# Optimization experiments

Measured on AMD Instinct MI355X. Metric: run time of the kernel, lower is better.

The kernel has to match this reference:

```python
import jax, jax.numpy as jnp
import numpy as np

B, S, E, H = 4, 2048, 1024, 16
D = E // H  # head_dim = 64

def setup_inputs() -> dict:
    key = jax.random.key(0)
    k1, k2, k3 = jax.random.split(key, 3)
    x = jax.random.normal(k1, (B, S, E), dtype=jnp.float32)
    # nn.Linear(E, 3E, bias=False): y = x @ W^T; we store W already transposed as [E, 3E]
    w_qkv = jax.random.normal(k2, (E, 3 * E), dtype=jnp.float32) * (E ** -0.5)
    w_out = jax.random.normal(k3, (E, E), dtype=jnp.float32) * (E ** -0.5)
    b_out = jnp.zeros((E,), dtype=jnp.float32)
    return {"x": x, "w_qkv": w_qkv, "w_out": w_out, "b_out": b_out}

def reference(x, w_qkv, w_out, b_out):
    b, s, e = x.shape
    h, d = H, e // H
    # qkv projection then rearrange 'b s (qkv h d) -> qkv b h s d'
    qkv = (x @ w_qkv).reshape(b, s, 3, h, d).transpose(2, 0, 3, 1, 4)
    q, k, v = qkv[0], qkv[1], qkv[2]            # each [b, h, s, d]
    scale = jnp.asarray(d, x.dtype) ** -0.5
    att = jnp.einsum('bhxd,bhyd->bhxy', q, k) * scale   # [b, h, s, s]
    att = jax.nn.softmax(att, axis=-1)
    o = jnp.einsum('bhxy,bhyd->bhxd', att, v)           # [b, h, s, d]
    o = o.transpose(0, 2, 1, 3).reshape(b, s, e)        # 'b h s d -> b s (h d)'
    return o @ w_out + b_out
```

## Files before the change

### kernel.cpp

```cpp
#include <hip/hip_runtime.h>
#include <cstdint>
#include <cstddef>


typedef __attribute__((ext_vector_type(8))) short short8;
typedef __attribute__((ext_vector_type(4))) float float4_;
typedef unsigned int u32;
typedef unsigned short u16;

__device__ __forceinline__ u16 f2b(float f) {
  u32 u = __float_as_uint(f);
  u += 0x7FFFu + ((u >> 16) & 1u);
  return (u16)(u >> 16);
}

__device__ __forceinline__ float fexp2(float x) {
#if __has_builtin(__builtin_amdgcn_exp2f)
  return __builtin_amdgcn_exp2f(x);
#else
  return exp2f(x);
#endif
}

__device__ __forceinline__ u32 pk_trunc(float lo, float hi) {
#if __has_builtin(__builtin_amdgcn_perm)
  return __builtin_amdgcn_perm(__float_as_uint(hi), __float_as_uint(lo), 0x07060302);
#else
  return (__float_as_uint(hi) & 0xFFFF0000u) | (__float_as_uint(lo) >> 16);
#endif
}

#if __has_builtin(__builtin_amdgcn_fdot2_f32_bf16)
typedef __bf16 bf16x2 __attribute__((ext_vector_type(2)));
__device__ __forceinline__ float accum_pk(u32 pk, float acc) {
  bf16x2 p = __builtin_bit_cast(bf16x2, pk);
  bf16x2 one = __builtin_bit_cast(bf16x2, (u32)0x3F803F80u);
  return __builtin_amdgcn_fdot2_f32_bf16(p, one, acc, false);
}
#else
__device__ __forceinline__ float accum_pk(u32 pk, float acc) {
  return acc + __uint_as_float(pk << 16) + __uint_as_float(pk & 0xFFFF0000u);
}
#endif

__device__ __forceinline__ void async_cp16(const void* g, void* l) {
  __builtin_amdgcn_global_load_lds(
      (const __attribute__((address_space(1))) u32*)g,
      (__attribute__((address_space(3))) u32*)l, 16, 0, 0);
}


__device__ __forceinline__ void transpose_block(const float* __restrict__ in,
                                                u16* __restrict__ out,
                                                int R, int C, int bx, int by,
                                                float t[32][33]) {
  int tx = threadIdx.x & 31, ty = threadIdx.x >> 5;
  int r0 = by * 32, c0 = bx * 32;
#pragma unroll
  for (int k = 0; k < 4; k++)
    t[ty + 8 * k][tx] = in[(size_t)(r0 + ty + 8 * k) * C + c0 + tx];
  __syncthreads();
#pragma unroll
  for (int k = 0; k < 4; k++)
    out[(size_t)(c0 + ty + 8 * k) * R + r0 + tx] = f2b(t[tx][ty + 8 * k]);
}

__global__ void prepass_kernel(const float* __restrict__ x, u16* __restrict__ Xb,
                               const float* __restrict__ wqkv, u16* __restrict__ Wqt,
                               const float* __restrict__ wout, u16* __restrict__ Wot) {
  __shared__ float t[32][33];
  int gid = blockIdx.x;
  if (gid < 8192) {
    int i = gid * 256 + threadIdx.x;
    float4 v = ((const float4*)x)[i];
    uint2 p;
    p.x = (u32)f2b(v.x) | ((u32)f2b(v.y) << 16);
    p.y = (u32)f2b(v.z) | ((u32)f2b(v.w) << 16);
    ((uint2*)Xb)[i] = p;
  } else if (gid < 11264) {
    int j = gid - 8192;
    transpose_block(wqkv, Wqt, 1024, 3072, j % 96, j / 96, t);
  } else {
    int j = gid - 11264;
    transpose_block(wout, Wot, 1024, 1024, j % 32, j / 32, t);
  }
}

__global__ void transpose_v(const u16* __restrict__ V, u16* __restrict__ Vt) {
  __shared__ u16 t[64][80];
  int bh = blockIdx.y, s0 = blockIdx.x * 64;
  const u16* Vh = V + (size_t)bh * 2048 * 64;
  u16* Vth = Vt + (size_t)bh * 64 * 2048;
  int tr = threadIdx.x >> 3;
  int tc = (threadIdx.x & 7) * 8;
#pragma unroll
  for (int p = 0; p < 2; p++) {
    int r = p * 32 + tr;
    *(uint4*)&t[r][tc] = *(const uint4*)(Vh + (size_t)(s0 + r) * 64 + tc);
  }
  __syncthreads();
#pragma unroll
  for (int p = 0; p < 2; p++) {
    int d = p * 32 + tr;
    u16 tmp[8];
#pragma unroll
    for (int k = 0; k < 8; k++) tmp[k] = t[tc + k][d];
    *(uint4*)(Vth + (size_t)d * 2048 + s0 + tc) = *(uint4*)tmp;
  }
}


__global__ __launch_bounds__(512, 2) void gemm_qkv_kernel(
    const u16* __restrict__ A, const u16* __restrict__ Bt,
    u16* __restrict__ QKV) {
  const int K = 1024;
  const int NT = 16;
  __shared__ short8 lA[2][2048];
  __shared__ short8 lB[2][2048];
  int tid = threadIdx.x;
  int wid = tid >> 6, l = tid & 63, lr = l & 15, lq = l >> 4;
  int wm = wid >> 2, wn = wid & 3;
  int gid = blockIdx.x;
  int xcd = gid & 7, j = gid >> 3;
  int nt = j % 12, mt = xcd * 4 + j / 12;
  int m0 = mt * 256, n0 = nt * 256;

  float4_ acc[8][4] = {};

  const u16* srcA[2][2];
  const u16* srcB[2][2];
#pragma unroll
  for (int h = 0; h < 2; h++)
#pragma unroll
    for (int s = 0; s < 2; s++) {
      int fl = h * 16 + s * 8 + (tid >> 6);
      int fr = fl >> 1, ks = fl & 1;
      srcA[h][s] = A + (size_t)(m0 + fr * 16 + lr) * K + ks * 32 + lq * 8;
      srcB[h][s] = Bt + (size_t)(n0 + fr * 16 + lr) * K + ks * 32 + lq * 8;
    }

  auto stageA = [&](int buf, int h, int k0) {
#pragma unroll
    for (int s = 0; s < 2; s++)
      async_cp16(srcA[h][s] + k0, &lA[buf][h * 1024 + s * 512 + tid]);
  };
  auto stageB = [&](int buf, int h, int k0) {
#pragma unroll
    for (int s = 0; s < 2; s++)
      async_cp16(srcB[h][s] + k0, &lB[buf][h * 1024 + s * 512 + tid]);
  };

  stageB(0, 0, 0); stageB(0, 1, 0);
  stageA(0, 0, 0); stageA(0, 1, 0);
  stageB(1, 0, 64); stageB(1, 1, 64);
  asm volatile("s_waitcnt vmcnt(4)" ::: "memory");
  __builtin_amdgcn_sched_barrier(0);
  __builtin_amdgcn_s_barrier();

  short8 areg[4], breg[4][2];
  for (int u = 0; u < NT; ++u) {
    int buf = u & 1, nbuf = buf ^ 1;
    int kA = (u < NT - 1 ? u + 1 : NT - 1) * 64;
    int kB = (u < NT - 2 ? u + 2 : NT - 1) * 64;

#pragma unroll
    for (int nf = 0; nf < 4; nf++) breg[nf][0] = lB[buf][((wn * 4 + nf) * 2 + 0) * 64 + l];
#pragma unroll
    for (int mf = 0; mf < 4; mf++) areg[mf] = lA[buf][((wm * 8 + mf) * 2 + 0) * 64 + l];
    stageA(nbuf, 0, kA);
    __builtin_amdgcn_s_barrier();
    asm volatile("s_waitcnt lgkmcnt(0)" ::: "memory");
    __builtin_amdgcn_sched_barrier(0);
    __builtin_amdgcn_s_setprio(1);
#pragma unroll
    for (int mf = 0; mf < 4; mf++)
#pragma unroll
      for (int nf = 0; nf < 4; nf++)
        acc[mf][nf] = __builtin_amdgcn_mfma_f32_16x16x32_bf16(areg[mf], breg[nf][0], acc[mf][nf], 0, 0, 0);
    __builtin_amdgcn_s_setprio(0);
    __builtin_amdgcn_s_barrier();

#pragma unroll
    for (int nf = 0; nf < 4; nf++) breg[nf][1] = lB[buf][((wn * 4 + nf) * 2 + 1) * 64 + l];
#pragma unroll
    for (int mf = 0; mf < 4; mf++) areg[mf] = lA[buf][((wm * 8 + 4 + mf) * 2 + 0) * 64 + l];
    stageA(nbuf, 1, kA);
    __builtin_amdgcn_s_barrier();
    asm volatile("s_waitcnt lgkmcnt(0)" ::: "memory");
    __builtin_amdgcn_sched_barrier(0);
    __builtin_amdgcn_s_setprio(1);
#pragma unroll
    for (int mf = 0; mf < 4; mf++)
#pragma unroll
      for (int nf = 0; nf < 4; nf++)
        acc[4 + mf][nf] = __builtin_amdgcn_mfma_f32_16x16x32_bf16(areg[mf], breg[nf][0], acc[4 + mf][nf], 0, 0, 0);
    __builtin_amdgcn_s_setprio(0);
    __builtin_amdgcn_s_barrier();

#pragma unroll
    for (int mf = 0; mf < 4; mf++) areg[mf] = lA[buf][((wm * 8 + mf) * 2 + 1) * 64 + l];
    stageB(buf, 0, kB);
    __builtin_amdgcn_s_barrier();
    asm volatile("s_waitcnt lgkmcnt(0)" ::: "memory");
    __builtin_amdgcn_sched_barrier(0);
    __builtin_amdgcn_s_setprio(1);
#pragma unroll
    for (int mf = 0; mf < 4; mf++)
#pragma unroll
      for (int nf = 0; nf < 4; nf++)
        acc[mf][nf] = __builtin_amdgcn_mfma_f32_16x16x32_bf16(areg[mf], breg[nf][1], acc[mf][nf], 0, 0, 0);
    __builtin_amdgcn_s_setprio(0);
    __builtin_amdgcn_s_barrier();

#pragma unroll
    for (int mf = 0; mf < 4; mf++) areg[mf] = lA[buf][((wm * 8 + 4 + mf) * 2 + 1) * 64 + l];
    stageB(buf, 1, kB);
    __builtin_amdgcn_s_barrier();
    asm volatile("s_waitcnt lgkmcnt(0)" ::: "memory");
    __builtin_amdgcn_sched_barrier(0);
    __builtin_amdgcn_s_setprio(1);
#pragma unroll
    for (int mf = 0; mf < 4; mf++)
#pragma unroll
      for (int nf = 0; nf < 4; nf++)
        acc[4 + mf][nf] = __builtin_amdgcn_mfma_f32_16x16x32_bf16(areg[mf], breg[nf][1], acc[4 + mf][nf], 0, 0, 0);
    __builtin_amdgcn_s_setprio(0);
    asm volatile("s_waitcnt vmcnt(4)" ::: "memory");
    __builtin_amdgcn_sched_barrier(0);
    __builtin_amdgcn_s_barrier();
  }
  asm volatile("s_waitcnt vmcnt(0)" ::: "memory");

  const float qsc = 0.18033688011112042f;
#pragma unroll
  for (int nf = 0; nf < 4; nf++) {
    int gn = n0 + wn * 64 + nf * 16 + lr;
    int sel = gn >> 10;
    int h = (gn >> 6) & 15;
    int d = gn & 63;
    float sc = (sel == 0) ? qsc : 1.0f;
    u16* dst = QKV + (size_t)sel * 8388608 + ((size_t)h * 2048) * 64 + d;
#pragma unroll
    for (int mf = 0; mf < 8; mf++) {
#pragma unroll
      for (int r = 0; r < 4; r++) {
        int gm = m0 + wm * 128 + mf * 16 + lq * 4 + r;
        int b = gm >> 11, s = gm & 2047;
        dst[((size_t)b * 16 * 2048 + s) * 64] = f2b(acc[mf][nf][r] * sc);
      }
    }
  }
}


__global__ __launch_bounds__(256) void gemm_out_kernel(
    const u16* __restrict__ A, const u16* __restrict__ Bt,
    const float* __restrict__ bias, float* __restrict__ out) {
  const int K = 1024;
  __shared__ short8 lA[2][512];
  __shared__ short8 lB[2][512];
  int tid = threadIdx.x;
  int w = tid >> 6, l = tid & 63, lr = l & 15, lq = l >> 4;
  int gid = blockIdx.x;
  int xcd = gid & 7, j = gid >> 3;
  int yloc = j & 7, xt = j >> 3;
  int m0 = (xcd * 8 + yloc) * 128, n0 = xt * 128;
  int wm = w & 1, wn = w >> 1;
  float4_ acc[4][4] = {};

  const u16* gA0 = A + (size_t)(m0 + w * 32 + lr) * K + lq * 8;
  const u16* gA1 = gA0 + 16 * K;
  const u16* gB0 = Bt + (size_t)(n0 + w * 32 + lr) * K + lq * 8;
  const u16* gB1 = gB0 + 16 * K;

  auto stage = [&](int buf, int k0) {
    async_cp16(gA0 + k0, &lA[buf][(w * 2 + 0) * 64 + l]);
    async_cp16(gA1 + k0, &lA[buf][(w * 2 + 1) * 64 + l]);
    async_cp16(gB0 + k0, &lB[buf][(w * 2 + 0) * 64 + l]);
    async_cp16(gB1 + k0, &lB[buf][(w * 2 + 1) * 64 + l]);
  };
  auto compute = [&](int buf) {
    short8 af[4], bf[4];
#pragma unroll
    for (int t = 0; t < 4; t++) {
      af[t] = lA[buf][(wm * 4 + t) * 64 + l];
      bf[t] = lB[buf][(wn * 4 + t) * 64 + l];
    }
#pragma unroll
    for (int mt = 0; mt < 4; mt++)
#pragma unroll
      for (int nt = 0; nt < 4; nt++)
        acc[mt][nt] = __builtin_amdgcn_mfma_f32_16x16x32_bf16(af[mt], bf[nt], acc[mt][nt], 0, 0, 0);
  };

  stage(0, 0);
  for (int k0 = 0; k0 < K; k0 += 64) {
    __syncthreads();
    stage(1, k0 + 32);
    compute(0);
    __syncthreads();
    if (k0 + 64 < K) stage(0, k0 + 64);
    compute(1);
  }

#pragma unroll
  for (int nt = 0; nt < 4; nt++) {
    int gn = n0 + wn * 64 + nt * 16 + lr;
    float bv = bias[gn];
#pragma unroll
    for (int mt = 0; mt < 4; mt++)
#pragma unroll
      for (int r = 0; r < 4; r++) {
        int gm = m0 + wm * 64 + mt * 16 + lq * 4 + r;
        out[(size_t)gm * 1024 + gn] = acc[mt][nt][r] + bv;
      }
  }
}


__global__ __launch_bounds__(256) void attn_kernel(
    const u16* __restrict__ Qb, const u16* __restrict__ Kb,
    const u16* __restrict__ Vt, u16* __restrict__ Ob) {
  const int S = 2048, D = 64;
  __shared__ short8 lK[2][512];
  __shared__ short8 lV[2][512];
  __shared__ __align__(16) u32 pb[4][16][20];
  int tid = threadIdx.x;
  int w = tid >> 6, l = tid & 63, lr = l & 15, lq = l >> 4;
  int gid = blockIdx.x;
  int xcd = gid & 7, j = gid >> 3;
  int bh = xcd * 8 + (j >> 4);
  int qblk = j & 15;
  int q0 = qblk * 128 + w * 32;
  const u16* Qh = Qb + (size_t)bh * S * D;
  const u16* Kh = Kb + (size_t)bh * S * D;
  const u16* Vh = Vt + (size_t)bh * D * S;

  short8 qf[2][2];
#pragma unroll
  for (int qg = 0; qg < 2; qg++) {
    qf[qg][0] = *(const short8*)(Qh + (q0 + qg * 16 + lr) * D + lq * 8);
    qf[qg][1] = *(const short8*)(Qh + (q0 + qg * 16 + lr) * D + 32 + lq * 8);
  }

  float ls[2][4] = {};
  float4_ o[2][4] = {};

  const u16* kg = Kh + (size_t)(((w >> 1) << 5) + 2 * lr + (w & 1)) * D + lq * 8;
  const u16* vg = Vh + (size_t)(w * 16 + lr) * S + lq * 8;

  auto stage = [&](int buf, int kv0) {
    async_cp16(kg + (size_t)kv0 * D, &lK[buf][(w * 2 + 0) * 64 + l]);
    async_cp16(kg + (size_t)kv0 * D + 32, &lK[buf][(w * 2 + 1) * 64 + l]);
    async_cp16(vg + kv0, &lV[buf][(w * 2 + 0) * 64 + l]);
    async_cp16(vg + kv0 + 32, &lV[buf][(w * 2 + 1) * 64 + l]);
  };

  auto compute = [&](int buf) {
#pragma unroll
    for (int sub = 0; sub < 2; sub++) {
      short8 ke0 = lK[buf][((sub * 2 + 0) * 2 + 0) * 64 + l];
      short8 ke1 = lK[buf][((sub * 2 + 0) * 2 + 1) * 64 + l];
      short8 ko0 = lK[buf][((sub * 2 + 1) * 2 + 0) * 64 + l];
      short8 ko1 = lK[buf][((sub * 2 + 1) * 2 + 1) * 64 + l];
#pragma unroll
      for (int qg = 0; qg < 2; qg++) {
        float4_ z = {0.f, 0.f, 0.f, 0.f};
        float4_ s0 = __builtin_amdgcn_mfma_f32_16x16x32_bf16(qf[qg][0], ke0, z, 0, 0, 0);
        s0 = __builtin_amdgcn_mfma_f32_16x16x32_bf16(qf[qg][1], ke1, s0, 0, 0, 0);
        float4_ s1 = __builtin_amdgcn_mfma_f32_16x16x32_bf16(qf[qg][0], ko0, z, 0, 0, 0);
        s1 = __builtin_amdgcn_mfma_f32_16x16x32_bf16(qf[qg][1], ko1, s1, 0, 0, 0);
#pragma unroll
        for (int r = 0; r < 4; r++) {
          float p0 = fexp2(s0[r]);
          float p1 = fexp2(s1[r]);
          u32 pk = pk_trunc(p0, p1);
          ls[qg][r] = accum_pk(pk, ls[qg][r]);
          pb[w][lq * 4 + r][lr] = pk;
        }
        short8 pa = *(const short8*)&pb[w][lr][lq * 4];
#pragma unroll
        for (int dt = 0; dt < 4; dt++)
          o[qg][dt] = __builtin_amdgcn_mfma_f32_16x16x32_bf16(
              pa, lV[buf][(dt * 2 + sub) * 64 + l], o[qg][dt], 0, 0, 0);
      }
    }
  };

  stage(0, 0);
  for (int kv0 = 0; kv0 < S; kv0 += 128) {
    __syncthreads();
    stage(1, kv0 + 64);
    compute(0);
    __syncthreads();
    if (kv0 + 128 < S) stage(0, kv0 + 128);
    compute(1);
  }

  int b = bh >> 4, h = bh & 15;
#pragma unroll
  for (int qg = 0; qg < 2; qg++) {
    float inv[4];
#pragma unroll
    for (int r = 0; r < 4; r++) {
      float s = ls[qg][r];
#pragma unroll
      for (int off = 1; off < 16; off <<= 1) s += __shfl_xor(s, off, 64);
      inv[r] = 1.0f / s;
    }
#pragma unroll
    for (int dt = 0; dt < 4; dt++)
#pragma unroll
      for (int r = 0; r < 4; r++) {
        int s_ = q0 + qg * 16 + lq * 4 + r;
        Ob[((size_t)(b * 2048 + s_)) * 1024 + h * 64 + dt * 16 + lr] =
            f2b(o[qg][dt][r] * inv[r]);
      }
  }
}


extern "C" void kernel_launch(void* const* d_in, const int* in_sizes, int n_in,
                              void* d_out, int out_size, void* d_ws, size_t ws_size,
                              hipStream_t stream) {
  const float* x     = (const float*)d_in[0];
  const float* w_qkv = (const float*)d_in[1];
  const float* w_out = (const float*)d_in[2];
  const float* b_out = (const float*)d_in[3];
  float* out = (float*)d_out;

  char* ws = (char*)d_ws;
  u16* Xb  = (u16*)(ws);
  u16* Wqt = (u16*)(ws + (16u << 20));
  u16* Wot = (u16*)(ws + (22u << 20));
  u16* QKV = (u16*)(ws + (24u << 20));
  u16* Qb  = QKV;
  u16* Kb  = QKV + 8388608;
  u16* Vb  = QKV + 16777216;
  u16* Vt  = (u16*)(ws + (72u << 20));
  u16* Ob  = Xb;

  prepass_kernel<<<12288, 256, 0, stream>>>(x, Xb, w_qkv, Wqt, w_out, Wot);
  gemm_qkv_kernel<<<384, 512, 0, stream>>>(Xb, Wqt, QKV);
  transpose_v<<<dim3(32, 64), 256, 0, stream>>>(Vb, Vt);
  attn_kernel<<<1024, 256, 0, stream>>>(Qb, Kb, Vt, Ob);
  gemm_out_kernel<<<512, 256, 0, stream>>>(Ob, Wot, b_out, out);
}
```

Baseline: 338.1 us.

## Shrink QKV GEMM tile to 128x256 and reuse its pipeline for output GEMM

The QKV projection GEMM drops from 256x256 to 128x256 tiles. Its grid doubles from 384 to 768 blocks, which gives better occupancy across the CUs. The pipeline now keeps a triple-buffered B tile and a double-buffered A tile, and some sched_barrier/lgkmcnt waits are removed. The output projection GEMM is rewritten onto the same 512-thread, 128x256-tile pipelined scheme, replacing the simpler 128x128 double-buffered loop. The trade-off is less operand reuse per block and more LDS traffic, in exchange for more parallelism and deeper prefetch.

```diff
diff --git a/kernel.cpp b/kernel.cpp
--- a/kernel.cpp
+++ b/kernel.cpp
@@ -115,118 +115,84 @@
     u16* __restrict__ QKV) {
   const int K = 1024;
   const int NT = 16;
-  __shared__ short8 lA[2][2048];
-  __shared__ short8 lB[2][2048];
+  __shared__ short8 lA[2][1024];
+  __shared__ short8 lB[3][2048];
   int tid = threadIdx.x;
   int wid = tid >> 6, l = tid & 63, lr = l & 15, lq = l >> 4;
   int wm = wid >> 2, wn = wid & 3;
   int gid = blockIdx.x;
   int xcd = gid & 7, j = gid >> 3;
-  int nt = j % 12, mt = xcd * 4 + j / 12;
-  int m0 = mt * 256, n0 = nt * 256;
-
-  float4_ acc[8][4] = {};
-
-  const u16* srcA[2][2];
-  const u16* srcB[2][2];
-#pragma unroll
-  for (int h = 0; h < 2; h++)
-#pragma unroll
-    for (int s = 0; s < 2; s++) {
-      int fl = h * 16 + s * 8 + (tid >> 6);
-      int fr = fl >> 1, ks = fl & 1;
-      srcA[h][s] = A + (size_t)(m0 + fr * 16 + lr) * K + ks * 32 + lq * 8;
-      srcB[h][s] = Bt + (size_t)(n0 + fr * 16 + lr) * K + ks * 32 + lq * 8;
-    }
-
-  auto stageA = [&](int buf, int h, int k0) {
+  int nt = j % 12, mt = xcd * 8 + j / 12;
+  int m0 = mt * 128, n0 = nt * 256;
+
+  float4_ acc[4][4] = {};
+
+  const u16* srcA[2];
+  const u16* srcB[4];
+#pragma unroll
+  for (int s = 0; s < 2; s++) {
+    int fl = s * 8 + wid;
+    srcA[s] = A + (size_t)(m0 + (fl >> 1) * 16 + lr) * K + (fl & 1) * 32 + lq * 8;
+  }
+#pragma unroll
+  for (int s = 0; s < 4; s++) {
+    int fl = s * 8 + wid;
+    srcB[s] = Bt + (size_t)(n0 + (fl >> 1) * 16 + lr) * K + (fl & 1) * 32 + lq * 8;
+  }
+
+  auto stageA = [&](int buf, int k0) {
 #pragma unroll
     for (int s = 0; s < 2; s++)
-      async_cp16(srcA[h][s] + k0, &lA[buf][h * 1024 + s * 512 + tid]);
-  };
-  auto stageB = [&](int buf, int h, int k0) {
-#pragma unroll
-    for (int s = 0; s < 2; s++)
-      async_cp16(srcB[h][s] + k0, &lB[buf][h * 1024 + s * 512 + tid]);
-  };
-
-  stageB(0, 0, 0); stageB(0, 1, 0);
-  stageA(0, 0, 0); stageA(0, 1, 0);
-  stageB(1, 0, 64); stageB(1, 1, 64);
+      async_cp16(srcA[s] + k0, &lA[buf][(s * 8 + wid) * 64 + l]);
+  };
+  auto stageB = [&](int bb, int k0) {
+#pragma unroll
+    for (int s = 0; s < 4; s++)
+      async_cp16(srcB[s] + k0, &lB[bb][(s * 8 + wid) * 64 + l]);
+  };
+
+  stageA(0, 0);
+  stageB(0, 0);
+  stageB(1, 64);
   asm volatile("s_waitcnt vmcnt(4)" ::: "memory");
-  __builtin_amdgcn_sched_barrier(0);
   __builtin_amdgcn_s_barrier();
 
-  short8 areg[4], breg[4][2];
   for (int u = 0; u < NT; ++u) {
-    int buf = u & 1, nbuf = buf ^ 1;
-    int kA = (u < NT - 1 ? u + 1 : NT - 1) * 64;
-    int kB = (u < NT - 2 ? u + 2 : NT - 1) * 64;
-
-#pragma unroll
-    for (int nf = 0; nf < 4; nf++) breg[nf][0] = lB[buf][((wn * 4 + nf) * 2 + 0) * 64 + l];
-#pragma unroll
-    for (int mf = 0; mf < 4; mf++) areg[mf] = lA[buf][((wm * 8 + mf) * 2 + 0) * 64 + l];
-    stageA(nbuf, 0, kA);
-    __builtin_amdgcn_s_barrier();
-    asm volatile("s_waitcnt lgkmcnt(0)" ::: "memory");
-    __builtin_amdgcn_sched_barrier(0);
+    int buf = u & 1;
+    int vb = u % 3;
+    int kA = (u + 1 < NT ? u + 1 : NT - 1) * 64;
+    int kB = (u + 2 < NT ? u + 2 : NT - 1) * 64;
+    short8 af[4], bf[4];
+
+#pragma unroll
+    for (int mf = 0; mf < 4; mf++) af[mf] = lA[buf][((wm * 4 + mf) * 2 + 0) * 64 + l];
+#pragma unroll
+    for (int nf = 0; nf < 4; nf++) bf[nf] = lB[vb][((wn * 4 + nf) * 2 + 0) * 64 + l];
+    stageA(buf ^ 1, kA);
+    __builtin_amdgcn_s_barrier();
     __builtin_amdgcn_s_setprio(1);
 #pragma unroll
     for (int mf = 0; mf < 4; mf++)
 #pragma unroll
       for (int nf = 0; nf < 4; nf++)
-        acc[mf][nf] = __builtin_amdgcn_mfma_f32_16x16x32_bf16(areg[mf], breg[nf][0], acc[mf][nf], 0, 0, 0);
+        acc[mf][nf] = __builtin_amdgcn_mfma_f32_16x16x32_bf16(af[mf], bf[nf], acc[mf][nf], 0, 0, 0);
     __builtin_amdgcn_s_setprio(0);
     __builtin_amdgcn_s_barrier();
 
 #pragma unroll
-    for (int nf = 0; nf < 4; nf++) breg[nf][1] = lB[buf][((wn * 4 + nf) * 2 + 1) * 64 + l];
-#pragma unroll
-    for (int mf = 0; mf < 4; mf++) areg[mf] = lA[buf][((wm * 8 + 4 + mf) * 2 + 0) * 64 + l];
-    stageA(nbuf, 1, kA);
-    __builtin_amdgcn_s_barrier();
-    asm volatile("s_waitcnt lgkmcnt(0)" ::: "memory");
-    __builtin_amdgcn_sched_barrier(0);
+    for (int mf = 0; mf < 4; mf++) af[mf] = lA[buf][((wm * 4 + mf) * 2 + 1) * 64 + l];
+#pragma unroll
+    for (int nf = 0; nf < 4; nf++) bf[nf] = lB[vb][((wn * 4 + nf) * 2 + 1) * 64 + l];
+    stageB((u + 2) % 3, kB);
+    __builtin_amdgcn_s_barrier();
     __builtin_amdgcn_s_setprio(1);
 #pragma unroll
     for (int mf = 0; mf < 4; mf++)
 #pragma unroll
       for (int nf = 0; nf < 4; nf++)
-        acc[4 + mf][nf] = __builtin_amdgcn_mfma_f32_16x16x32_bf16(areg[mf], breg[nf][0], acc[4 + mf][nf], 0, 0, 0);
-    __builtin_amdgcn_s_setprio(0);
-    __builtin_amdgcn_s_barrier();
-
-#pragma unroll
-    for (int mf = 0; mf < 4; mf++) areg[mf] = lA[buf][((wm * 8 + mf) * 2 + 1) * 64 + l];
-    stageB(buf, 0, kB);
-    __builtin_amdgcn_s_barrier();
-    asm volatile("s_waitcnt lgkmcnt(0)" ::: "memory");
-    __builtin_amdgcn_sched_barrier(0);
-    __builtin_amdgcn_s_setprio(1);
-#pragma unroll
-    for (int mf = 0; mf < 4; mf++)
-#pragma unroll
-      for (int nf = 0; nf < 4; nf++)
-        acc[mf][nf] = __builtin_amdgcn_mfma_f32_16x16x32_bf16(areg[mf], breg[nf][1], acc[mf][nf], 0, 0, 0);
-    __builtin_amdgcn_s_setprio(0);
-    __builtin_amdgcn_s_barrier();
-
-#pragma unroll
-    for (int mf = 0; mf < 4; mf++) areg[mf] = lA[buf][((wm * 8 + 4 + mf) * 2 + 1) * 64 + l];
-    stageB(buf, 1, kB);
-    __builtin_amdgcn_s_barrier();
-    asm volatile("s_waitcnt lgkmcnt(0)" ::: "memory");
-    __builtin_amdgcn_sched_barrier(0);
-    __builtin_amdgcn_s_setprio(1);
-#pragma unroll
-    for (int mf = 0; mf < 4; mf++)
-#pragma unroll
-      for (int nf = 0; nf < 4; nf++)
-        acc[4 + mf][nf] = __builtin_amdgcn_mfma_f32_16x16x32_bf16(areg[mf], breg[nf][1], acc[4 + mf][nf], 0, 0, 0);
+        acc[mf][nf] = __builtin_amdgcn_mfma_f32_16x16x32_bf16(af[mf], bf[nf], acc[mf][nf], 0, 0, 0);
     __builtin_amdgcn_s_setprio(0);
     asm volatile("s_waitcnt vmcnt(4)" ::: "memory");
-    __builtin_amdgcn_sched_barrier(0);
     __builtin_amdgcn_s_barrier();
   }
   asm volatile("s_waitcnt vmcnt(0)" ::: "memory");
@@ -241,10 +207,10 @@
     float sc = (sel == 0) ? qsc : 1.0f;
     u16* dst = QKV + (size_t)sel * 8388608 + ((size_t)h * 2048) * 64 + d;
 #pragma unroll
-    for (int mf = 0; mf < 8; mf++) {
+    for (int mf = 0; mf < 4; mf++) {
 #pragma unroll
       for (int r = 0; r < 4; r++) {
-        int gm = m0 + wm * 128 + mf * 16 + lq * 4 + r;
+        int gm = m0 + wm * 64 + mf * 16 + lq * 4 + r;
         int b = gm >> 11, s = gm & 2047;
         dst[((size_t)b * 16 * 2048 + s) * 64] = f2b(acc[mf][nf][r] * sc);
       }
@@ -253,66 +219,103 @@
 }
 
 
-__global__ __launch_bounds__(256) void gemm_out_kernel(
+__global__ __launch_bounds__(512, 2) void gemm_out_kernel(
     const u16* __restrict__ A, const u16* __restrict__ Bt,
     const float* __restrict__ bias, float* __restrict__ out) {
   const int K = 1024;
-  __shared__ short8 lA[2][512];
-  __shared__ short8 lB[2][512];
+  const int NT = 16;
+  __shared__ short8 lA[2][1024];
+  __shared__ short8 lB[3][2048];
   int tid = threadIdx.x;
-  int w = tid >> 6, l = tid & 63, lr = l & 15, lq = l >> 4;
+  int wid = tid >> 6, l = tid & 63, lr = l & 15, lq = l >> 4;
+  int wm = wid >> 2, wn = wid & 3;
   int gid = blockIdx.x;
   int xcd = gid & 7, j = gid >> 3;
-  int yloc = j & 7, xt = j >> 3;
-  int m0 = (xcd * 8 + yloc) * 128, n0 = xt * 128;
-  int wm = w & 1, wn = w >> 1;
+  int nt = j % 4, mt = xcd * 8 + j / 4;
+  int m0 = mt * 128, n0 = nt * 256;
+
   float4_ acc[4][4] = {};
 
-  const u16* gA0 = A + (size_t)(m0 + w * 32 + lr) * K + lq * 8;
-  const u16* gA1 = gA0 + 16 * K;
-  const u16* gB0 = Bt + (size_t)(n0 + w * 32 + lr) * K + lq * 8;
-  const u16* gB1 = gB0 + 16 * K;
-
-  auto stage = [&](int buf, int k0) {
-    async_cp16(gA0 + k0, &lA[buf][(w * 2 + 0) * 64 + l]);
-    async_cp16(gA1 + k0, &lA[buf][(w * 2 + 1) * 64 + l]);
-    async_cp16(gB0 + k0, &lB[buf][(w * 2 + 0) * 64 + l]);
-    async_cp16(gB1 + k0, &lB[buf][(w * 2 + 1) * 64 + l]);
-  };
-  auto compute = [&](int buf) {
+  const u16* srcA[2];
+  const u16* srcB[4];
+#pragma unroll
+  for (int s = 0; s < 2; s++) {
+    int fl = s * 8 + wid;
+    srcA[s] = A + (size_t)(m0 + (fl >> 1) * 16 + lr) * K + (fl & 1) * 32 + lq * 8;
+  }
+#pragma unroll
+  for (int s = 0; s < 4; s++) {
+    int fl = s * 8 + wid;
+    srcB[s] = Bt + (size_t)(n0 + (fl >> 1) * 16 + lr) * K + (fl & 1) * 32 + lq * 8;
+  }
+
+  auto stageA = [&](int buf, int k0) {
+#pragma unroll
+    for (int s = 0; s < 2; s++)
+      async_cp16(srcA[s] + k0, &lA[buf][(s * 8 + wid) * 64 + l]);
+  };
+  auto stageB = [&](int bb, int k0) {
+#pragma unroll
+    for (int s = 0; s < 4; s++)
+      async_cp16(srcB[s] + k0, &lB[bb][(s * 8 + wid) * 64 + l]);
+  };
+
+  stageA(0, 0);
+  stageB(0, 0);
+  stageB(1, 64);
+  asm volatile("s_waitcnt vmcnt(4)" ::: "memory");
+  __builtin_amdgcn_s_barrier();
+
+  for (int u = 0; u < NT; ++u) {
+    int buf = u & 1;
+    int vb = u % 3;
+    int kA = (u + 1 < NT ? u + 1 : NT - 1) * 64;
+    int kB = (u + 2 < NT ? u + 2 : NT - 1) * 64;
     short8 af[4], bf[4];
-#pragma unroll
-    for (int t = 0; t < 4; t++) {
-      af[t] = lA[buf][(wm * 4 + t) * 64 + l];
-      bf[t] = lB[buf][(wn * 4 + t) * 64 + l];
-    }
-#pragma unroll
-    for (int mt = 0; mt < 4; mt++)
-#pragma unroll
-      for (int nt = 0; nt < 4; nt++)
-        acc[mt][nt] = __builtin_amdgcn_mfma_f32_16x16x32_bf16(af[mt], bf[nt], acc[mt][nt], 0, 0, 0);
-  };
-
-  stage(0, 0);
-  for (int k0 = 0; k0 < K; k0 += 64) {
-    __syncthreads();
-    stage(1, k0 + 32);
-    compute(0);
-    __syncthreads();
-    if (k0 + 64 < K) stage(0, k0 + 64);
-    compute(1);
-  }
-
-#pragma unroll
-  for (int nt = 0; nt < 4; nt++) {
-    int gn = n0 + wn * 64 + nt * 16 + lr;
+
+#pragma unroll
+    for (int mf = 0; mf < 4; mf++) af[mf] = lA[buf][((wm * 4 + mf) * 2 + 0) * 64 + l];
+#pragma unroll
+    for (int nf = 0; nf < 4; nf++) bf[nf] = lB[vb][((wn * 4 + nf) * 2 + 0) * 64 + l];
+    stageA(buf ^ 1, kA);
+    __builtin_amdgcn_s_barrier();
+    __builtin_amdgcn_s_setprio(1);
+#pragma unroll
+    for (int mf = 0; mf < 4; mf++)
+#pragma unroll
+      for (int nf = 0; nf < 4; nf++)
+        acc[mf][nf] = __builtin_amdgcn_mfma_f32_16x16x32_bf16(af[mf], bf[nf], acc[mf][nf], 0, 0, 0);
+    __builtin_amdgcn_s_setprio(0);
+    __builtin_amdgcn_s_barrier();
+
+#pragma unroll
+    for (int mf = 0; mf < 4; mf++) af[mf] = lA[buf][((wm * 4 + mf) * 2 + 1) * 64 + l];
+#pragma unroll
+    for (int nf = 0; nf < 4; nf++) bf[nf] = lB[vb][((wn * 4 + nf) * 2 + 1) * 64 + l];
+    stageB((u + 2) % 3, kB);
+    __builtin_amdgcn_s_barrier();
+    __builtin_amdgcn_s_setprio(1);
+#pragma unroll
+    for (int mf = 0; mf < 4; mf++)
+#pragma unroll
+      for (int nf = 0; nf < 4; nf++)
+        acc[mf][nf] = __builtin_amdgcn_mfma_f32_16x16x32_bf16(af[mf], bf[nf], acc[mf][nf], 0, 0, 0);
+    __builtin_amdgcn_s_setprio(0);
+    asm volatile("s_waitcnt vmcnt(4)" ::: "memory");
+    __builtin_amdgcn_s_barrier();
+  }
+  asm volatile("s_waitcnt vmcnt(0)" ::: "memory");
+
+#pragma unroll
+  for (int nf = 0; nf < 4; nf++) {
+    int gn = n0 + wn * 64 + nf * 16 + lr;
     float bv = bias[gn];
 #pragma unroll
-    for (int mt = 0; mt < 4; mt++)
+    for (int mf = 0; mf < 4; mf++)
 #pragma unroll
       for (int r = 0; r < 4; r++) {
-        int gm = m0 + wm * 64 + mt * 16 + lq * 4 + r;
-        out[(size_t)gm * 1024 + gn] = acc[mt][nt][r] + bv;
+        int gm = m0 + wm * 64 + mf * 16 + lq * 4 + r;
+        out[(size_t)gm * 1024 + gn] = acc[mf][nf][r] + bv;
       }
   }
 }
@@ -441,8 +444,8 @@
   u16* Ob  = Xb;
 
   prepass_kernel<<<12288, 256, 0, stream>>>(x, Xb, w_qkv, Wqt, w_out, Wot);
-  gemm_qkv_kernel<<<384, 512, 0, stream>>>(Xb, Wqt, QKV);
+  gemm_qkv_kernel<<<768, 512, 0, stream>>>(Xb, Wqt, QKV);
   transpose_v<<<dim3(32, 64), 256, 0, stream>>>(Vb, Vt);
   attn_kernel<<<1024, 256, 0, stream>>>(Qb, Kb, Vt, Ob);
-  gemm_out_kernel<<<512, 256, 0, stream>>>(Ob, Wot, b_out, out);
-}
+  gemm_out_kernel<<<256, 512, 0, stream>>>(Ob, Wot, b_out, out);
+}
```

New measurement: 342.5 us. Within noise of the previous version (+1.3%).
